# Kernel optimization log

Measured on AMD Instinct MI355X. Metric: run time of the kernel, lower is better.

The kernel has to match this reference:

```python
import jax, jax.numpy as jnp
import numpy as np

B, C, F, N = 2, 8, 80, 128
H, W = 512, 1024


def setup_inputs() -> dict:
    key = jax.random.key(0)
    k1, k2, k3 = jax.random.split(key, 3)
    x = jax.random.normal(k1, (B, C, F, N, N), dtype=jnp.float32)
    quad = jax.random.randint(k2, (H, W), 0, F, dtype=jnp.int32)
    # uv buffer holds coordinates already scaled into [0, N-1]
    uv = jax.random.uniform(k3, (H, W, 2), dtype=jnp.float32) * (N - 1)
    return {"x": x, "quad": quad, "uv": uv}


def reference(x, quad, uv):
    """x: B x C x F x N x N texture patches; quad: H x W face indices;
    uv: H x W x 2 in-patch coordinates in [0, N-1]. Returns B x C x H x W."""
    Bx, Cx, Fx, Nx, _ = x.shape
    Hh, Ww = quad.shape
    u = uv[..., 0].reshape(-1)  # HW
    v = uv[..., 1].reshape(-1)
    u0 = jnp.clip(jnp.floor(u), 0, Nx - 2).astype(jnp.int32)
    v0 = jnp.clip(jnp.floor(v), 0, Nx - 2).astype(jnp.int32)
    du = u - u0.astype(u.dtype)
    dv = v - v0.astype(v.dtype)
    base = quad.reshape(-1).astype(jnp.int32) * (Nx * Nx)  # HW
    x_flat = x.reshape(Bx, Cx, Fx * Nx * Nx)
    i00 = base + v0 * Nx + u0
    g00 = x_flat[:, :, i00]           # B x C x HW
    g01 = x_flat[:, :, i00 + 1]
    g10 = x_flat[:, :, i00 + Nx]
    g11 = x_flat[:, :, i00 + Nx + 1]
    w00 = (1.0 - du) * (1.0 - dv)
    w01 = du * (1.0 - dv)
    w10 = (1.0 - du) * dv
    w11 = du * dv
    out = g00 * w00 + g01 * w01 + g10 * w10 + g11 * w11  # B x C x HW
    return out.reshape(Bx, Cx, Hh, Ww)
```

## Files before the change

### kernel.cpp

```cpp
#include <hip/hip_runtime.h>
#include <hip/hip_fp16.h>

#define BC   16
#define FD   80
#define ND   128
#define NN   (ND * ND)
#define HW   (512 * 1024)
#define HW_SHIFT 19

#define YH_BYTES ((size_t)FD * NN * BC * sizeof(__half))

__global__ __launch_bounds__(256)
void repack_kernel(const float* __restrict__ x, __half* __restrict__ y)
{
    const int fv  = blockIdx.x;
    const int f   = fv >> 7;
    const int v   = fv & (ND - 1);
    const int tid = threadIdx.x;

    __shared__ float lds[ND * 17];

#pragma unroll
    for (int r = 0; r < 2; ++r) {
        const int i4 = tid + r * 256;
        const int c  = i4 >> 5;
        const int u4 = i4 & 31;
        const float4 val = *(const float4*)(
            x + (((size_t)c * FD + f) * ND + v) * ND + u4 * 4);
        lds[(u4 * 4 + 0) * 17 + c] = val.x;
        lds[(u4 * 4 + 1) * 17 + c] = val.y;
        lds[(u4 * 4 + 2) * 17 + c] = val.z;
        lds[(u4 * 4 + 3) * 17 + c] = val.w;
    }
    __syncthreads();

    const int u  = tid >> 1;
    const int c0 = (tid & 1) * 8;
    uint4 r;
    unsigned* rp = (unsigned*)&r;
#pragma unroll
    for (int j = 0; j < 4; ++j) {
        const __half2 h = __floats2half2_rn(lds[u * 17 + c0 + 2 * j],
                                            lds[u * 17 + c0 + 2 * j + 1]);
        rp[j] = *(const unsigned*)&h;
    }
    uint4* y4 = (uint4*)(y + (size_t)fv * ND * BC);
    y4[tid] = r;
}

__device__ inline void acc8(float* o, uint4 t, float w)
{
    const unsigned* p = (const unsigned*)&t;
#pragma unroll
    for (int j = 0; j < 4; ++j) {
        const float2 fp = __half22float2(*(const __half2*)&p[j]);
        o[2 * j + 0] += fp.x * w;
        o[2 * j + 1] += fp.y * w;
    }
}

__global__ __launch_bounds__(256)
void gather_kernel(const __half* __restrict__ y,
                   const int*    __restrict__ quad,
                   const float2* __restrict__ uv2,
                   float* __restrict__ out)
{
    const int pix = blockIdx.x * 256 + threadIdx.x;

    const float2 t = uv2[pix];
    const int    f = quad[pix];

    const float u = t.x;
    const float v = t.y;

    int u0 = (int)floorf(u);
    int v0 = (int)floorf(v);
    u0 = min(max(u0, 0), ND - 2);
    v0 = min(max(v0, 0), ND - 2);

    const size_t base = (((size_t)f * ND + v0) * ND + u0) * BC;
    const uint4* r0 = (const uint4*)(y + base);
    const uint4* r1 = (const uint4*)(y + base + (size_t)ND * BC);
    const uint4 a0 = r0[0], a1 = r0[1];
    const uint4 b0 = r0[2], b1 = r0[3];
    const uint4 c0 = r1[0], c1 = r1[1];
    const uint4 d0 = r1[2], d1 = r1[3];

    const float du = u - (float)u0;
    const float dv = v - (float)v0;
    const float w00 = (1.0f - du) * (1.0f - dv);
    const float w01 = du * (1.0f - dv);
    const float w10 = (1.0f - du) * dv;
    const float w11 = du * dv;

    float o[BC];
#pragma unroll
    for (int c = 0; c < BC; ++c) o[c] = 0.0f;

    acc8(o,     a0, w00); acc8(o + 8, a1, w00);
    acc8(o,     b0, w01); acc8(o + 8, b1, w01);
    acc8(o,     c0, w10); acc8(o + 8, c1, w10);
    acc8(o,     d0, w11); acc8(o + 8, d1, w11);

#pragma unroll
    for (int c = 0; c < BC; ++c)
        __builtin_nontemporal_store(o[c], &out[(size_t)c * HW + pix]);
}

__global__ __launch_bounds__(256)
void resample_fallback_kernel(const float* __restrict__ x,
                              const int*   __restrict__ quad,
                              const float2* __restrict__ uv2,
                              float* __restrict__ out)
{
    const int gid = blockIdx.x * 256 + threadIdx.x;
    const int pix = gid & (HW - 1);
    const int bc  = gid >> HW_SHIFT;

    const float2 t = uv2[pix];
    const int    f = quad[pix];

    const float u = t.x;
    const float v = t.y;

    int u0 = (int)floorf(u);
    int v0 = (int)floorf(v);
    u0 = min(max(u0, 0), ND - 2);
    v0 = min(max(v0, 0), ND - 2);

    const float du = u - (float)u0;
    const float dv = v - (float)v0;

    const float w00 = (1.0f - du) * (1.0f - dv);
    const float w01 = du * (1.0f - dv);
    const float w10 = (1.0f - du) * dv;
    const float w11 = du * dv;

    const float* p = x + ((size_t)bc * FD + (size_t)f) * NN + v0 * ND + u0;
    out[gid] = p[0] * w00 + p[1] * w01 + p[ND] * w10 + p[ND + 1] * w11;
}

extern "C" void kernel_launch(void* const* d_in, const int* in_sizes, int n_in,
                              void* d_out, int out_size, void* d_ws, size_t ws_size,
                              hipStream_t stream)
{
    const float*  x    = (const float*)d_in[0];
    const int*    quad = (const int*)d_in[1];
    const float2* uv2  = (const float2*)d_in[2];
    float*        out  = (float*)d_out;

    if (ws_size >= YH_BYTES) {
        __half* y = (__half*)d_ws;
        repack_kernel<<<FD * ND, 256, 0, stream>>>(x, y);
        gather_kernel<<<HW / 256, 256, 0, stream>>>(y, quad, uv2, out);
    } else {
        const int total = BC * HW;
        resample_fallback_kernel<<<total / 256, 256, 0, stream>>>(x, quad, uv2, out);
    }
}
```

Measured before the change: 167.2 us.

## Duplicate half texture into even/odd shifted copies for aligned 64-byte gathers

The repack kernel now writes two fp16 copies of the channel-interleaved texture, the second shifted by one texel, so every bilinear horizontal pair starts at an even slot and forms one aligned 64-byte chunk. The gather kernel picks the copy from the parity of u0, so the two-texel loads per row no longer straddle cache-line or sector boundaries. The repack also drops its LDS transpose in favour of per-thread strided channel loads with direct 32-byte stores. The cost is twice the workspace and repack write traffic, and a larger footprint for the gather to cache.

```diff
diff --git a/kernel.cpp b/kernel.cpp
--- a/kernel.cpp
+++ b/kernel.cpp
@@ -8,44 +8,41 @@
 #define HW   (512 * 1024)
 #define HW_SHIFT 19
 
-#define YH_BYTES ((size_t)FD * NN * BC * sizeof(__half))
+#define COPY_HALVES ((size_t)FD * NN * BC)
+#define Z_BYTES     (2 * COPY_HALVES * sizeof(__half))
 
 __global__ __launch_bounds__(256)
-void repack_kernel(const float* __restrict__ x, __half* __restrict__ y)
+void repack_kernel(const float* __restrict__ x, __half* __restrict__ z)
 {
-    const int fv  = blockIdx.x;
-    const int f   = fv >> 7;
-    const int v   = fv & (ND - 1);
-    const int tid = threadIdx.x;
+    const int gid = blockIdx.x * 256 + threadIdx.x;
+    const int u   = gid & (ND - 1);
+    const int fv  = gid >> 7;
 
-    __shared__ float lds[ND * 17];
+    const size_t texel = (size_t)fv * ND + u;
 
+    float g[BC];
 #pragma unroll
-    for (int r = 0; r < 2; ++r) {
-        const int i4 = tid + r * 256;
-        const int c  = i4 >> 5;
-        const int u4 = i4 & 31;
-        const float4 val = *(const float4*)(
-            x + (((size_t)c * FD + f) * ND + v) * ND + u4 * 4);
-        lds[(u4 * 4 + 0) * 17 + c] = val.x;
-        lds[(u4 * 4 + 1) * 17 + c] = val.y;
-        lds[(u4 * 4 + 2) * 17 + c] = val.z;
-        lds[(u4 * 4 + 3) * 17 + c] = val.w;
+    for (int c = 0; c < BC; ++c)
+        g[c] = x[(size_t)c * ((size_t)FD * NN) + texel];
+
+    unsigned hp[8];
+#pragma unroll
+    for (int j = 0; j < 8; ++j) {
+        const __half2 h = __floats2half2_rn(g[2 * j], g[2 * j + 1]);
+        hp[j] = *(const unsigned*)&h;
     }
-    __syncthreads();
+    const uint4 h0 = make_uint4(hp[0], hp[1], hp[2], hp[3]);
+    const uint4 h1 = make_uint4(hp[4], hp[5], hp[6], hp[7]);
 
-    const int u  = tid >> 1;
-    const int c0 = (tid & 1) * 8;
-    uint4 r;
-    unsigned* rp = (unsigned*)&r;
-#pragma unroll
-    for (int j = 0; j < 4; ++j) {
-        const __half2 h = __floats2half2_rn(lds[u * 17 + c0 + 2 * j],
-                                            lds[u * 17 + c0 + 2 * j + 1]);
-        rp[j] = *(const unsigned*)&h;
+    __half* r0 = z + (size_t)fv * (ND * BC) + (size_t)u * BC;
+    *(uint4*)(r0)     = h0;
+    *(uint4*)(r0 + 8) = h1;
+
+    if (u > 0) {
+        __half* r1 = z + COPY_HALVES + (size_t)fv * (ND * BC) + (size_t)(u - 1) * BC;
+        *(uint4*)(r1)     = h0;
+        *(uint4*)(r1 + 8) = h1;
     }
-    uint4* y4 = (uint4*)(y + (size_t)fv * ND * BC);
-    y4[tid] = r;
 }
 
 __device__ inline void acc8(float* o, uint4 t, float w)
@@ -60,7 +57,7 @@
 }
 
 __global__ __launch_bounds__(256)
-void gather_kernel(const __half* __restrict__ y,
+void gather_kernel(const __half* __restrict__ z,
                    const int*    __restrict__ quad,
                    const float2* __restrict__ uv2,
                    float* __restrict__ out)
@@ -78,9 +75,13 @@
     u0 = min(max(u0, 0), ND - 2);
     v0 = min(max(v0, 0), ND - 2);
 
-    const size_t base = (((size_t)f * ND + v0) * ND + u0) * BC;
-    const uint4* r0 = (const uint4*)(y + base);
-    const uint4* r1 = (const uint4*)(y + base + (size_t)ND * BC);
+    const int p    = u0 & 1;
+    const int slot = u0 - p;
+
+    const size_t base = ((((size_t)p * FD + f) * ND + v0) * ND + slot) * BC;
+    const uint4* r0 = (const uint4*)(z + base);
+    const uint4* r1 = (const uint4*)(z + base + (size_t)ND * BC);
+
     const uint4 a0 = r0[0], a1 = r0[1];
     const uint4 b0 = r0[2], b1 = r0[3];
     const uint4 c0 = r1[0], c1 = r1[1];
@@ -149,10 +150,11 @@
     const float2* uv2  = (const float2*)d_in[2];
     float*        out  = (float*)d_out;
 
-    if (ws_size >= YH_BYTES) {
-        __half* y = (__half*)d_ws;
-        repack_kernel<<<FD * ND, 256, 0, stream>>>(x, y);
-        gather_kernel<<<HW / 256, 256, 0, stream>>>(y, quad, uv2, out);
+    if (ws_size >= Z_BYTES) {
+        __half* z = (__half*)d_ws;
+        const int texels = FD * ND * ND;
+        repack_kernel<<<texels / 256, 256, 0, stream>>>(x, z);
+        gather_kernel<<<HW / 256, 256, 0, stream>>>(z, quad, uv2, out);
     } else {
         const int total = BC * HW;
         resample_fallback_kernel<<<total / 256, 256, 0, stream>>>(x, quad, uv2, out);
```

Result: slower. 172.5 us (+3.2%).
